# Performance work log

Measured on AMD Instinct MI355X. Metric: run time of the kernel, lower is better.

## Reference

```python
import jax, jax.numpy as jnp
import numpy as np

L = 160        # voxel grid side
BATCH = 4
N_SAMPLE = 62500
N = 64


def _build_coords():
    rng = np.random.default_rng(0)
    coords = []
    for b in range(BATCH):
        c = np.unique(rng.integers(0, L, (N_SAMPLE, 3)), axis=0)  # sorted, unique
        bc = np.concatenate([np.full((len(c), 1), b, dtype=np.int64), c.astype(np.int64)], axis=1)
        coords.append(bc)
    return np.concatenate(coords, axis=0)  # [P,4] = (batch, x, y, z), globally key-sorted


def _neighbor_table(C):
    # integer key per coordinate; coords are unique+sorted so keys are strictly increasing
    keys = ((C[:, 0] * L + C[:, 1]) * L + C[:, 2]) * L + C[:, 3]
    P = C.shape[0]
    offs = np.array([[dx, dy, dz] for dx in (-1, 0, 1) for dy in (-1, 0, 1) for dz in (-1, 0, 1)], dtype=np.int64)
    nbr = np.full((P, 27), -1, dtype=np.int32)
    for k, o in enumerate(offs):
        nc = C[:, 1:] + o
        valid = np.all((nc >= 0) & (nc < L), axis=1)
        nk = ((C[:, 0] * L + nc[:, 0]) * L + nc[:, 1]) * L + nc[:, 2]
        pos = np.clip(np.searchsorted(keys, nk), 0, P - 1)
        found = valid & (keys[pos] == nk)
        nbr[:, k] = np.where(found, pos, -1).astype(np.int32)
    return nbr


def setup_inputs() -> dict:
    C = _build_coords()
    nbr = _neighbor_table(C)
    P = C.shape[0]
    key = jax.random.key(0)
    ks = jax.random.split(key, 10)
    s = 0.05  # small weight scale keeps activations well-conditioned
    return {
        "feats": jax.random.normal(ks[0], (P, N), jnp.float32),
        "cond": jax.random.normal(ks[1], (P, 2 * N), jnp.float32),
        "W1a": jax.random.normal(ks[2], (27, N, N), jnp.float32) * s,
        "b1a": jax.random.normal(ks[3], (N,), jnp.float32) * s,
        "W1b": jax.random.normal(ks[4], (27, N, N), jnp.float32) * s,
        "b1b": jax.random.normal(ks[5], (N,), jnp.float32) * s,
        "W2a": jax.random.normal(ks[6], (27, N, N), jnp.float32) * s,
        "b2a": jax.random.normal(ks[7], (N,), jnp.float32) * s,
        "W2b": jax.random.normal(ks[8], (27, N, N), jnp.float32) * s,
        "b2b": jax.random.normal(ks[9], (N,), jnp.float32) * s,
        "nbr": jnp.asarray(nbr),
    }


def _sparse_conv(x, nbr, W, b):
    # x: [P,N] features, nbr: [P,27] neighbor indices (-1 = missing)
    mask = (nbr >= 0)
    idx = jnp.maximum(nbr, 0)
    acc0 = jnp.zeros((x.shape[0], W.shape[2]), x.dtype)

    def body(acc, kin):
        wk, ik, mk = kin            # wk:[N,N], ik:[P], mk:[P]
        g = x[ik] * mk[:, None].astype(x.dtype)
        return acc + g @ wk, None

    out, _ = jax.lax.scan(body, acc0, (W, idx.T, mask.T))
    return out + b


def reference(feats, cond, W1a, b1a, W1b, b1b, W2a, b2a, W2b, b2b, nbr):
    x_res = feats
    # conv_1: conv -> relu -> conv
    h = _sparse_conv(feats, nbr, W1a, b1a)
    h = jax.nn.relu(h)
    h = _sparse_conv(h, nbr, W1b, b1b)
    # FiLM from condition (features_at_coordinates at identical coords -> direct lookup)
    beta, gamma = jnp.split(cond, 2, axis=1)
    h = h * beta + gamma
    # conv_2: conv -> relu -> conv -> relu
    h = _sparse_conv(h, nbr, W2a, b2a)
    h = jax.nn.relu(h)
    h = _sparse_conv(h, nbr, W2b, b2b)
    h = jax.nn.relu(h)
    # residual: x_res at same coordinates is an identity lookup
    return h + x_res
```

## Files before the change

### kernel.cpp

```cpp
#include <hip/hip_runtime.h>
#include <hip/hip_bf16.h>


#define N 64
#define TAPS 27
#define MT 256

typedef unsigned short u16;
typedef __attribute__((ext_vector_type(8))) short short8;
typedef __attribute__((ext_vector_type(16))) float floatx16;

__device__ __forceinline__ float bf2f(u16 v) {
    union { unsigned u; float f; } c;
    c.u = ((unsigned)v) << 16;
    return c.f;
}
__device__ __forceinline__ u16 f2bf(float f) {
    __hip_bfloat16 h = __float2bfloat16(f);
    u16 r;
    __builtin_memcpy(&r, &h, 2);
    return r;
}
__device__ __forceinline__ void split2(float x, u16& hi, u16& lo) {
    hi = f2bf(x);
    lo = f2bf(x - bf2f(hi));
}

__device__ __forceinline__ void async16(u16* lds, const u16* g) {
    __builtin_amdgcn_global_load_lds(
        (const __attribute__((address_space(1))) unsigned int*)g,
        (__attribute__((address_space(3))) unsigned int*)lds, 16, 0, 0);
}

__global__ void zero_zp(u16* zp) { zp[threadIdx.x] = 0; }

__global__ void split_feats(const float* __restrict__ x, u16* __restrict__ hl, int n) {
    int i = blockIdx.x * 256 + threadIdx.x;
    if (i >= n) return;
    int p = i >> 6, c = i & 63;
    u16 h, l;
    split2(x[i], h, l);
    hl[(size_t)p * 128 + c] = h;
    hl[(size_t)p * 128 + 64 + c] = l;
}

__global__ void transpose_w(const float* __restrict__ W, u16* __restrict__ Wt) {
    const float* src = W + blockIdx.x * (N * N);
    u16* dst = Wt + blockIdx.x * (N * 128);
    int t = threadIdx.x;
#pragma unroll
    for (int m = 0; m < 16; ++m) {
        int e = t + m * 256;
        int i = e >> 6;
        int j = e & 63;
        u16 h, l;
        split2(src[e], h, l);
        int x = (((i >> 3) ^ (j & 7)) * 8) + (i & 7);
        dst[j * 128 + x] = h;
        dst[j * 128 + 64 + x] = l;
    }
}

template <int MODE>
__global__ __launch_bounds__(256, 2) void conv_k(
    const u16* __restrict__ Xhl, const u16* __restrict__ Wt,
    const float* __restrict__ bias, const int* __restrict__ nbr,
    const float* __restrict__ cond, const float* __restrict__ resid,
    const u16* __restrict__ zp,
    u16* __restrict__ out_hl, float* __restrict__ out_f32, int P) {
    __shared__ __align__(16) u16 As[MT * 128];
    __shared__ __align__(16) u16 Bs[N * 128];

    const int tid = threadIdx.x;
    const int pbase = blockIdx.x * MT;

    const int w = tid >> 6;
    const int lane = tid & 63;
    const int cn = lane & 31;
    const int kh = lane >> 5;
    const int rowA0 = w * 64 + cn;

    const int lrow = lane >> 4;
    const int lslot = lane & 15;
    const int swzE = (lslot >> 3) * 64 + (((lslot & 7) ^ lrow) * 8);
    const int swzO = (lslot >> 3) * 64 + (((lslot & 7) ^ (4 + lrow)) * 8);

    floatx16 acc00, acc01, acc10, acc11;
#pragma unroll
    for (int i = 0; i < 16; ++i) { acc00[i] = 0.f; acc01[i] = 0.f; acc10[i] = 0.f; acc11[i] = 0.f; }

    for (int k = 0; k < TAPS; ++k) {
        if (k) __syncthreads();

        int ii[16];
#pragma unroll
        for (int i = 0; i < 16; ++i) {
            const int pr = pbase + w * 64 + i * 4 + lrow;
            const int pc = (pr < P) ? pr : (P - 1);
            int v = nbr[(size_t)pc * TAPS + k];
            ii[i] = (pr < P) ? v : -1;
        }
#pragma unroll
        for (int i = 0; i < 16; ++i) {
            const u16* s = (ii[i] >= 0)
                ? Xhl + (size_t)ii[i] * 128 + ((i & 1) ? swzO : swzE)
                : zp + lslot * 8;
            async16(&As[(w * 64 + i * 4) * 128], s);
        }
        {
            const u16* wk = Wt + ((size_t)k * N + w * 16) * 128 + lane * 8;
#pragma unroll
            for (int q = 0; q < 4; ++q) {
                async16(&Bs[(w * 16 + q * 4) * 128], wk + q * (4 * 128));
            }
        }

        __syncthreads();

#pragma unroll
        for (int kc = 0; kc < 4; ++kc) {
            const int g = 2 * kc + kh;
            const int sw = (g ^ (cn & 7)) * 8;
            const short8 a_h0 = *reinterpret_cast<const short8*>(&As[rowA0 * 128 + sw]);
            const short8 a_l0 = *reinterpret_cast<const short8*>(&As[rowA0 * 128 + 64 + sw]);
            const short8 a_h1 = *reinterpret_cast<const short8*>(&As[(rowA0 + 32) * 128 + sw]);
            const short8 a_l1 = *reinterpret_cast<const short8*>(&As[(rowA0 + 32) * 128 + 64 + sw]);
            const short8 b_h0 = *reinterpret_cast<const short8*>(&Bs[cn * 128 + sw]);
            const short8 b_l0 = *reinterpret_cast<const short8*>(&Bs[cn * 128 + 64 + sw]);
            const short8 b_h1 = *reinterpret_cast<const short8*>(&Bs[(cn + 32) * 128 + sw]);
            const short8 b_l1 = *reinterpret_cast<const short8*>(&Bs[(cn + 32) * 128 + 64 + sw]);

            acc00 = __builtin_amdgcn_mfma_f32_32x32x16_bf16(a_h0, b_h0, acc00, 0, 0, 0);
            acc00 = __builtin_amdgcn_mfma_f32_32x32x16_bf16(a_h0, b_l0, acc00, 0, 0, 0);
            acc00 = __builtin_amdgcn_mfma_f32_32x32x16_bf16(a_l0, b_h0, acc00, 0, 0, 0);

            acc01 = __builtin_amdgcn_mfma_f32_32x32x16_bf16(a_h0, b_h1, acc01, 0, 0, 0);
            acc01 = __builtin_amdgcn_mfma_f32_32x32x16_bf16(a_h0, b_l1, acc01, 0, 0, 0);
            acc01 = __builtin_amdgcn_mfma_f32_32x32x16_bf16(a_l0, b_h1, acc01, 0, 0, 0);

            acc10 = __builtin_amdgcn_mfma_f32_32x32x16_bf16(a_h1, b_h0, acc10, 0, 0, 0);
            acc10 = __builtin_amdgcn_mfma_f32_32x32x16_bf16(a_h1, b_l0, acc10, 0, 0, 0);
            acc10 = __builtin_amdgcn_mfma_f32_32x32x16_bf16(a_l1, b_h0, acc10, 0, 0, 0);

            acc11 = __builtin_amdgcn_mfma_f32_32x32x16_bf16(a_h1, b_h1, acc11, 0, 0, 0);
            acc11 = __builtin_amdgcn_mfma_f32_32x32x16_bf16(a_h1, b_l1, acc11, 0, 0, 0);
            acc11 = __builtin_amdgcn_mfma_f32_32x32x16_bf16(a_l1, b_h1, acc11, 0, 0, 0);
        }
    }

    auto epi = [&](const floatx16& a, int mt, int nt) {
        const int j = nt * 32 + cn;
        const float bj = bias[j];
#pragma unroll
        for (int reg = 0; reg < 16; ++reg) {
            const int row = (reg & 3) + 8 * (reg >> 2) + 4 * kh;
            const int p = pbase + w * 64 + mt * 32 + row;
            if (p < P) {
                float o = a[reg] + bj;
                if (MODE == 0 || MODE == 2) o = fmaxf(o, 0.f);
                if (MODE == 1) {
                    const float be = cond[(size_t)p * (2 * N) + j];
                    const float ga = cond[(size_t)p * (2 * N) + N + j];
                    o = o * be + ga;
                }
                if (MODE == 3) {
                    o = fmaxf(o, 0.f) + resid[(size_t)p * N + j];
                    out_f32[(size_t)p * N + j] = o;
                } else {
                    u16 h, l;
                    split2(o, h, l);
                    out_hl[(size_t)p * 128 + j] = h;
                    out_hl[(size_t)p * 128 + 64 + j] = l;
                }
            }
        }
    };
    epi(acc00, 0, 0);
    epi(acc01, 0, 1);
    epi(acc10, 1, 0);
    epi(acc11, 1, 1);
}

extern "C" void kernel_launch(void* const* d_in, const int* in_sizes, int n_in,
                              void* d_out, int out_size, void* d_ws, size_t ws_size,
                              hipStream_t stream) {
    const float* feats = (const float*)d_in[0];
    const float* cond  = (const float*)d_in[1];
    const float* W1a   = (const float*)d_in[2];
    const float* b1a   = (const float*)d_in[3];
    const float* W1b   = (const float*)d_in[4];
    const float* b1b   = (const float*)d_in[5];
    const float* W2a   = (const float*)d_in[6];
    const float* b2a   = (const float*)d_in[7];
    const float* W2b   = (const float*)d_in[8];
    const float* b2b   = (const float*)d_in[9];
    const int* nbr     = (const int*)d_in[10];
    float* out = (float*)d_out;
    u16* out_hl = (u16*)d_out;

    const int P = in_sizes[0] / N;

    const size_t wtElems = (size_t)TAPS * N * 128;
    u16* zp  = (u16*)d_ws;
    u16* wt0 = zp + 128;
    u16* wt1 = wt0 + wtElems;
    u16* wt2 = wt1 + wtElems;
    u16* wt3 = wt2 + wtElems;
    u16* hA  = wt3 + wtElems;

    zero_zp<<<1, 128, 0, stream>>>(zp);
    transpose_w<<<TAPS, 256, 0, stream>>>(W1a, wt0);
    transpose_w<<<TAPS, 256, 0, stream>>>(W1b, wt1);
    transpose_w<<<TAPS, 256, 0, stream>>>(W2a, wt2);
    transpose_w<<<TAPS, 256, 0, stream>>>(W2b, wt3);
    split_feats<<<(P * N + 255) / 256, 256, 0, stream>>>(feats, out_hl, P * N);

    const int blocks = (P + MT - 1) / MT;
    conv_k<0><<<blocks, 256, 0, stream>>>(out_hl, wt0, b1a, nbr, nullptr, nullptr, zp, hA, nullptr, P);
    conv_k<1><<<blocks, 256, 0, stream>>>(hA, wt1, b1b, nbr, cond, nullptr, zp, out_hl, nullptr, P);
    conv_k<2><<<blocks, 256, 0, stream>>>(out_hl, wt2, b2a, nbr, nullptr, nullptr, zp, hA, nullptr, P);
    conv_k<3><<<blocks, 256, 0, stream>>>(hA, wt3, b2b, nbr, nullptr, feats, zp, nullptr, out, P);
}
```

Measured before the change: 1.116 ms.

## Replace dense 27-tap gather with rulebook sparse pairs plus dense center tap

```diff
diff --git a/kernel.cpp b/kernel.cpp
--- a/kernel.cpp
+++ b/kernel.cpp
@@ -4,7 +4,9 @@
 
 #define N 64
 #define TAPS 27
-#define MT 256
+#define MTD 128
+#define MT2 128
+#define SEGCAP 8192
 
 typedef unsigned short u16;
 typedef __attribute__((ext_vector_type(8))) short short8;
@@ -25,14 +27,26 @@
     hi = f2bf(x);
     lo = f2bf(x - bf2f(hi));
 }
-
 __device__ __forceinline__ void async16(u16* lds, const u16* g) {
     __builtin_amdgcn_global_load_lds(
         (const __attribute__((address_space(1))) unsigned int*)g,
         (__attribute__((address_space(3))) unsigned int*)lds, 16, 0, 0);
 }
 
-__global__ void zero_zp(u16* zp) { zp[threadIdx.x] = 0; }
+__global__ void zero_misc(u16* zp, int* hdr) {
+    const int t = threadIdx.x;
+    zp[t] = 0;
+    if (t < 64) hdr[t] = 0;
+}
+
+__global__ void zero_partial(float* p, const unsigned char* __restrict__ hasSp, int P) {
+    long i = (long)blockIdx.x * 256 + threadIdx.x;
+    const long n4 = (long)P * 16;
+    const long stride = (long)gridDim.x * 256;
+    const float4 z = make_float4(0.f, 0.f, 0.f, 0.f);
+    for (; i < n4; i += stride)
+        if (hasSp[i >> 4]) reinterpret_cast<float4*>(p)[i] = z;
+}
 
 __global__ void split_feats(const float* __restrict__ x, u16* __restrict__ hl, int n) {
     int i = blockIdx.x * 256 + threadIdx.x;
@@ -44,9 +58,12 @@
     hl[(size_t)p * 128 + 64 + c] = l;
 }
 
-__global__ void transpose_w(const float* __restrict__ W, u16* __restrict__ Wt) {
-    const float* src = W + blockIdx.x * (N * N);
-    u16* dst = Wt + blockIdx.x * (N * 128);
+__global__ void transpose_w4(const float* __restrict__ A, const float* __restrict__ B,
+                             const float* __restrict__ C, const float* __restrict__ D,
+                             u16* __restrict__ Wt) {
+    const float* srcs[4] = {A, B, C, D};
+    const float* src = srcs[blockIdx.y] + blockIdx.x * (N * N);
+    u16* dst = Wt + (size_t)blockIdx.y * (TAPS * N * 128) + (size_t)blockIdx.x * (N * 128);
     int t = threadIdx.x;
 #pragma unroll
     for (int m = 0; m < 16; ++m) {
@@ -61,124 +78,240 @@
     }
 }
 
-template <int MODE>
-__global__ __launch_bounds__(256, 2) void conv_k(
+__global__ void build_pairs(const int* __restrict__ nbr, int* __restrict__ hdr,
+                            int* __restrict__ pair_p, int* __restrict__ pair_q,
+                            unsigned char* __restrict__ hasSp, int P) {
+    int p = blockIdx.x * 256 + threadIdx.x;
+    if (p >= P) return;
+    const int* row = nbr + (size_t)p * TAPS;
+    int hs = 0;
+#pragma unroll
+    for (int k = 0; k < TAPS; ++k) {
+        if (k == 13) continue;
+        int q = row[k];
+        if (q >= 0) {
+            hs = 1;
+            int pos = atomicAdd(&hdr[k], 1);
+            if (pos < SEGCAP) {
+                pair_p[k * SEGCAP + pos] = p;
+                pair_q[k * SEGCAP + pos] = q;
+            }
+        }
+    }
+    hasSp[p] = (unsigned char)hs;
+}
+
+__global__ void finalize_pairs(int* __restrict__ hdr, int* __restrict__ c2k,
+                               int* __restrict__ cbase,
+                               int* __restrict__ pair_p, int* __restrict__ pair_q) {
+    __shared__ int soff[28];
+    const int tid = threadIdx.x;
+    if (tid == 0) {
+        int tot = 0;
+        for (int k = 0; k < TAPS; ++k) {
+            int c = hdr[k];
+            if (c > SEGCAP) c = SEGCAP;
+            hdr[k] = c;
+            soff[k] = tot;
+            tot += (c + MT2 - 1) / MT2;
+        }
+        soff[27] = tot;
+        hdr[32] = tot;
+    }
+    __syncthreads();
+    const int tot = soff[27];
+    for (int idx = tid; idx < tot; idx += 256) {
+        int k = 0;
+        while (!(idx >= soff[k] && idx < soff[k + 1])) ++k;
+        c2k[idx] = k;
+        cbase[idx] = k * SEGCAP + (idx - soff[k]) * MT2;
+    }
+    for (int k = 0; k < TAPS; ++k) {
+        const int c = hdr[k];
+        const int e = ((c + MT2 - 1) / MT2) * MT2;
+        for (int j = c + tid; j < e; j += 256) {
+            pair_p[k * SEGCAP + j] = 0;
+            pair_q[k * SEGCAP + j] = -1;
+        }
+    }
+}
+
+__global__ __launch_bounds__(256, 3) void sparse_k(
     const u16* __restrict__ Xhl, const u16* __restrict__ Wt,
-    const float* __restrict__ bias, const int* __restrict__ nbr,
-    const float* __restrict__ cond, const float* __restrict__ resid,
-    const u16* __restrict__ zp,
-    u16* __restrict__ out_hl, float* __restrict__ out_f32, int P) {
-    __shared__ __align__(16) u16 As[MT * 128];
+    const int* __restrict__ pair_p, const int* __restrict__ pair_q,
+    const int* __restrict__ c2k, const int* __restrict__ cbase,
+    const int* __restrict__ hdr, const u16* __restrict__ zp,
+    float* __restrict__ partial) {
+    __shared__ __align__(16) u16 As[MT2 * 128];
     __shared__ __align__(16) u16 Bs[N * 128];
+    __shared__ int pp[MT2];
 
     const int tid = threadIdx.x;
-    const int pbase = blockIdx.x * MT;
-
     const int w = tid >> 6;
     const int lane = tid & 63;
     const int cn = lane & 31;
     const int kh = lane >> 5;
-    const int rowA0 = w * 64 + cn;
-
     const int lrow = lane >> 4;
     const int lslot = lane & 15;
     const int swzE = (lslot >> 3) * 64 + (((lslot & 7) ^ lrow) * 8);
     const int swzO = (lslot >> 3) * 64 + (((lslot & 7) ^ (4 + lrow)) * 8);
-
-    floatx16 acc00, acc01, acc10, acc11;
-#pragma unroll
-    for (int i = 0; i < 16; ++i) { acc00[i] = 0.f; acc01[i] = 0.f; acc10[i] = 0.f; acc11[i] = 0.f; }
-
-    for (int k = 0; k < TAPS; ++k) {
-        if (k) __syncthreads();
-
-        int ii[16];
-#pragma unroll
-        for (int i = 0; i < 16; ++i) {
-            const int pr = pbase + w * 64 + i * 4 + lrow;
-            const int pc = (pr < P) ? pr : (P - 1);
-            int v = nbr[(size_t)pc * TAPS + k];
-            ii[i] = (pr < P) ? v : -1;
-        }
-#pragma unroll
-        for (int i = 0; i < 16; ++i) {
-            const u16* s = (ii[i] >= 0)
-                ? Xhl + (size_t)ii[i] * 128 + ((i & 1) ? swzO : swzE)
-                : zp + lslot * 8;
-            async16(&As[(w * 64 + i * 4) * 128], s);
+    const int rowA = w * 32 + cn;
+
+    const int tc = hdr[32];
+    for (int c = blockIdx.x; c < tc; c += gridDim.x) {
+        if (c != (int)blockIdx.x) __syncthreads();
+        const int k = c2k[c];
+        const int base = cbase[c];
+
+        if (tid < MT2) pp[tid] = pair_p[base + tid];
+#pragma unroll
+        for (int i = 0; i < 8; ++i) {
+            const int q = pair_q[base + w * 32 + i * 4 + lrow];
+            const u16* s = (q >= 0) ? Xhl + (size_t)q * 128 + ((i & 1) ? swzO : swzE)
+                                    : zp + lslot * 8;
+            async16(&As[(w * 32 + i * 4) * 128], s);
         }
         {
             const u16* wk = Wt + ((size_t)k * N + w * 16) * 128 + lane * 8;
 #pragma unroll
-            for (int q = 0; q < 4; ++q) {
-                async16(&Bs[(w * 16 + q * 4) * 128], wk + q * (4 * 128));
-            }
-        }
-
+            for (int q = 0; q < 4; ++q)
+                async16(&Bs[(w * 16 + q * 4) * 128], wk + q * 512);
+        }
         __syncthreads();
 
+        floatx16 acc0, acc1;
+#pragma unroll
+        for (int i = 0; i < 16; ++i) { acc0[i] = 0.f; acc1[i] = 0.f; }
 #pragma unroll
         for (int kc = 0; kc < 4; ++kc) {
             const int g = 2 * kc + kh;
             const int sw = (g ^ (cn & 7)) * 8;
-            const short8 a_h0 = *reinterpret_cast<const short8*>(&As[rowA0 * 128 + sw]);
-            const short8 a_l0 = *reinterpret_cast<const short8*>(&As[rowA0 * 128 + 64 + sw]);
-            const short8 a_h1 = *reinterpret_cast<const short8*>(&As[(rowA0 + 32) * 128 + sw]);
-            const short8 a_l1 = *reinterpret_cast<const short8*>(&As[(rowA0 + 32) * 128 + 64 + sw]);
+            const short8 a_h = *reinterpret_cast<const short8*>(&As[rowA * 128 + sw]);
+            const short8 a_l = *reinterpret_cast<const short8*>(&As[rowA * 128 + 64 + sw]);
             const short8 b_h0 = *reinterpret_cast<const short8*>(&Bs[cn * 128 + sw]);
             const short8 b_l0 = *reinterpret_cast<const short8*>(&Bs[cn * 128 + 64 + sw]);
             const short8 b_h1 = *reinterpret_cast<const short8*>(&Bs[(cn + 32) * 128 + sw]);
             const short8 b_l1 = *reinterpret_cast<const short8*>(&Bs[(cn + 32) * 128 + 64 + sw]);
-
-            acc00 = __builtin_amdgcn_mfma_f32_32x32x16_bf16(a_h0, b_h0, acc00, 0, 0, 0);
-            acc00 = __builtin_amdgcn_mfma_f32_32x32x16_bf16(a_h0, b_l0, acc00, 0, 0, 0);
-            acc00 = __builtin_amdgcn_mfma_f32_32x32x16_bf16(a_l0, b_h0, acc00, 0, 0, 0);
-
-            acc01 = __builtin_amdgcn_mfma_f32_32x32x16_bf16(a_h0, b_h1, acc01, 0, 0, 0);
-            acc01 = __builtin_amdgcn_mfma_f32_32x32x16_bf16(a_h0, b_l1, acc01, 0, 0, 0);
-            acc01 = __builtin_amdgcn_mfma_f32_32x32x16_bf16(a_l0, b_h1, acc01, 0, 0, 0);
-
-            acc10 = __builtin_amdgcn_mfma_f32_32x32x16_bf16(a_h1, b_h0, acc10, 0, 0, 0);
-            acc10 = __builtin_amdgcn_mfma_f32_32x32x16_bf16(a_h1, b_l0, acc10, 0, 0, 0);
-            acc10 = __builtin_amdgcn_mfma_f32_32x32x16_bf16(a_l1, b_h0, acc10, 0, 0, 0);
-
-            acc11 = __builtin_amdgcn_mfma_f32_32x32x16_bf16(a_h1, b_h1, acc11, 0, 0, 0);
-            acc11 = __builtin_amdgcn_mfma_f32_32x32x16_bf16(a_h1, b_l1, acc11, 0, 0, 0);
-            acc11 = __builtin_amdgcn_mfma_f32_32x32x16_bf16(a_l1, b_h1, acc11, 0, 0, 0);
-        }
-    }
-
-    auto epi = [&](const floatx16& a, int mt, int nt) {
-        const int j = nt * 32 + cn;
-        const float bj = bias[j];
+            acc0 = __builtin_amdgcn_mfma_f32_32x32x16_bf16(a_h, b_h0, acc0, 0, 0, 0);
+            acc0 = __builtin_amdgcn_mfma_f32_32x32x16_bf16(a_h, b_l0, acc0, 0, 0, 0);
+            acc0 = __builtin_amdgcn_mfma_f32_32x32x16_bf16(a_l, b_h0, acc0, 0, 0, 0);
+            acc1 = __builtin_amdgcn_mfma_f32_32x32x16_bf16(a_h, b_h1, acc1, 0, 0, 0);
+            acc1 = __builtin_amdgcn_mfma_f32_32x32x16_bf16(a_h, b_l1, acc1, 0, 0, 0);
+            acc1 = __builtin_amdgcn_mfma_f32_32x32x16_bf16(a_l, b_h1, acc1, 0, 0, 0);
+        }
 #pragma unroll
         for (int reg = 0; reg < 16; ++reg) {
             const int row = (reg & 3) + 8 * (reg >> 2) + 4 * kh;
-            const int p = pbase + w * 64 + mt * 32 + row;
-            if (p < P) {
-                float o = a[reg] + bj;
-                if (MODE == 0 || MODE == 2) o = fmaxf(o, 0.f);
-                if (MODE == 1) {
-                    const float be = cond[(size_t)p * (2 * N) + j];
-                    const float ga = cond[(size_t)p * (2 * N) + N + j];
-                    o = o * be + ga;
-                }
-                if (MODE == 3) {
-                    o = fmaxf(o, 0.f) + resid[(size_t)p * N + j];
-                    out_f32[(size_t)p * N + j] = o;
-                } else {
-                    u16 h, l;
-                    split2(o, h, l);
-                    out_hl[(size_t)p * 128 + j] = h;
-                    out_hl[(size_t)p * 128 + 64 + j] = l;
-                }
-            }
-        }
-    };
-    epi(acc00, 0, 0);
-    epi(acc01, 0, 1);
-    epi(acc10, 1, 0);
-    epi(acc11, 1, 1);
+            const int p = pp[w * 32 + row];
+            unsafeAtomicAdd(&partial[(size_t)p * N + cn], acc0[reg]);
+            unsafeAtomicAdd(&partial[(size_t)p * N + 32 + cn], acc1[reg]);
+        }
+    }
+}
+
+template <int MODE>
+__global__ __launch_bounds__(256, 3) void conv_dense(
+    const u16* Xhl, const u16* __restrict__ Wt13,
+    const float* __restrict__ bias, const float* __restrict__ cond,
+    const float* __restrict__ resid, const u16* __restrict__ zp,
+    const unsigned char* __restrict__ hasSp,
+    float* partial, u16* out_hl, float* out_f32, int P) {
+    __shared__ __align__(16) u16 As[MTD * 128];
+    __shared__ __align__(16) u16 Bs[N * 128];
+
+    const int tid = threadIdx.x;
+    const int pbase = blockIdx.x * MTD;
+    const int w = tid >> 6;
+    const int lane = tid & 63;
+    const int cn = lane & 31;
+    const int kh = lane >> 5;
+    const int lrow = lane >> 4;
+    const int lslot = lane & 15;
+    const int swzE = (lslot >> 3) * 64 + (((lslot & 7) ^ lrow) * 8);
+    const int swzO = (lslot >> 3) * 64 + (((lslot & 7) ^ (4 + lrow)) * 8);
+    const int rowA = w * 32 + cn;
+
+#pragma unroll
+    for (int i = 0; i < 8; ++i) {
+        const int pr = pbase + w * 32 + i * 4 + lrow;
+        const u16* s = (pr < P) ? Xhl + (size_t)pr * 128 + ((i & 1) ? swzO : swzE)
+                                : zp + lslot * 8;
+        async16(&As[(w * 32 + i * 4) * 128], s);
+    }
+    {
+        const u16* wk = Wt13 + (size_t)(w * 16) * 128 + lane * 8;
+#pragma unroll
+        for (int q = 0; q < 4; ++q)
+            async16(&Bs[(w * 16 + q * 4) * 128], wk + q * 512);
+    }
+    __syncthreads();
+
+    floatx16 acc0, acc1;
+#pragma unroll
+    for (int i = 0; i < 16; ++i) { acc0[i] = 0.f; acc1[i] = 0.f; }
+
+#pragma unroll
+    for (int kc = 0; kc < 4; ++kc) {
+        const int g = 2 * kc + kh;
+        const int sw = (g ^ (cn & 7)) * 8;
+        const short8 a_h = *reinterpret_cast<const short8*>(&As[rowA * 128 + sw]);
+        const short8 a_l = *reinterpret_cast<const short8*>(&As[rowA * 128 + 64 + sw]);
+        const short8 b_h0 = *reinterpret_cast<const short8*>(&Bs[cn * 128 + sw]);
+        const short8 b_l0 = *reinterpret_cast<const short8*>(&Bs[cn * 128 + 64 + sw]);
+        const short8 b_h1 = *reinterpret_cast<const short8*>(&Bs[(cn + 32) * 128 + sw]);
+        const short8 b_l1 = *reinterpret_cast<const short8*>(&Bs[(cn + 32) * 128 + 64 + sw]);
+        acc0 = __builtin_amdgcn_mfma_f32_32x32x16_bf16(a_h, b_h0, acc0, 0, 0, 0);
+        acc0 = __builtin_amdgcn_mfma_f32_32x32x16_bf16(a_h, b_l0, acc0, 0, 0, 0);
+        acc0 = __builtin_amdgcn_mfma_f32_32x32x16_bf16(a_l, b_h0, acc0, 0, 0, 0);
+        acc1 = __builtin_amdgcn_mfma_f32_32x32x16_bf16(a_h, b_h1, acc1, 0, 0, 0);
+        acc1 = __builtin_amdgcn_mfma_f32_32x32x16_bf16(a_h, b_l1, acc1, 0, 0, 0);
+        acc1 = __builtin_amdgcn_mfma_f32_32x32x16_bf16(a_l, b_h1, acc1, 0, 0, 0);
+    }
+
+#pragma unroll
+    for (int reg = 0; reg < 16; ++reg) {
+        const int row = (reg & 3) + 8 * (reg >> 2) + 4 * kh;
+        const int p = pbase + w * 32 + row;
+        if (p < P && hasSp[p]) {
+            acc0[reg] += partial[(size_t)p * N + cn];
+            acc1[reg] += partial[(size_t)p * N + 32 + cn];
+        }
+    }
+    __syncthreads();
+
+    const float bj0 = bias[cn];
+    const float bj1 = bias[32 + cn];
+#pragma unroll
+    for (int reg = 0; reg < 16; ++reg) {
+        const int row = (reg & 3) + 8 * (reg >> 2) + 4 * kh;
+        const int p = pbase + w * 32 + row;
+        if (p >= P) continue;
+        float o0 = acc0[reg] + bj0;
+        float o1 = acc1[reg] + bj1;
+        if (MODE == 0 || MODE == 2) { o0 = fmaxf(o0, 0.f); o1 = fmaxf(o1, 0.f); }
+        if (MODE == 1) {
+            const float be0 = cond[(size_t)p * 128 + cn];
+            const float ga0 = cond[(size_t)p * 128 + 64 + cn];
+            const float be1 = cond[(size_t)p * 128 + 32 + cn];
+            const float ga1 = cond[(size_t)p * 128 + 96 + cn];
+            o0 = o0 * be0 + ga0;
+            o1 = o1 * be1 + ga1;
+        }
+        if (MODE == 3) {
+            o0 = fmaxf(o0, 0.f) + resid[(size_t)p * N + cn];
+            o1 = fmaxf(o1, 0.f) + resid[(size_t)p * N + 32 + cn];
+            out_f32[(size_t)p * N + cn] = o0;
+            out_f32[(size_t)p * N + 32 + cn] = o1;
+        } else {
+            u16 h, l;
+            split2(o0, h, l);
+            out_hl[(size_t)p * 128 + cn] = h;
+            out_hl[(size_t)p * 128 + 64 + cn] = l;
+            split2(o1, h, l);
+            out_hl[(size_t)p * 128 + 32 + cn] = h;
+            out_hl[(size_t)p * 128 + 96 + cn] = l;
+        }
+    }
 }
 
 extern "C" void kernel_launch(void* const* d_in, const int* in_sizes, int n_in,
@@ -195,29 +328,55 @@
     const float* W2b   = (const float*)d_in[8];
     const float* b2b   = (const float*)d_in[9];
     const int* nbr     = (const int*)d_in[10];
-    float* out = (float*)d_out;
-    u16* out_hl = (u16*)d_out;
 
     const int P = in_sizes[0] / N;
-
-    const size_t wtElems = (size_t)TAPS * N * 128;
-    u16* zp  = (u16*)d_ws;
-    u16* wt0 = zp + 128;
-    u16* wt1 = wt0 + wtElems;
-    u16* wt2 = wt1 + wtElems;
-    u16* wt3 = wt2 + wtElems;
-    u16* hA  = wt3 + wtElems;
-
-    zero_zp<<<1, 128, 0, stream>>>(zp);
-    transpose_w<<<TAPS, 256, 0, stream>>>(W1a, wt0);
-    transpose_w<<<TAPS, 256, 0, stream>>>(W1b, wt1);
-    transpose_w<<<TAPS, 256, 0, stream>>>(W2a, wt2);
-    transpose_w<<<TAPS, 256, 0, stream>>>(W2b, wt3);
-    split_feats<<<(P * N + 255) / 256, 256, 0, stream>>>(feats, out_hl, P * N);
-
-    const int blocks = (P + MT - 1) / MT;
-    conv_k<0><<<blocks, 256, 0, stream>>>(out_hl, wt0, b1a, nbr, nullptr, nullptr, zp, hA, nullptr, P);
-    conv_k<1><<<blocks, 256, 0, stream>>>(hA, wt1, b1b, nbr, cond, nullptr, zp, out_hl, nullptr, P);
-    conv_k<2><<<blocks, 256, 0, stream>>>(out_hl, wt2, b2a, nbr, nullptr, nullptr, zp, hA, nullptr, P);
-    conv_k<3><<<blocks, 256, 0, stream>>>(hA, wt3, b2b, nbr, nullptr, feats, zp, nullptr, out, P);
-}
+    const size_t wtE = (size_t)TAPS * N * 128;
+
+    char* ws = (char*)d_ws;
+    u16* zp = (u16*)ws;        ws += 512;
+    u16* wt = (u16*)ws;        ws += 4 * wtE * sizeof(u16);
+    int* hdr = (int*)ws;       ws += 256;
+    int* c2k = (int*)ws;       ws += 2048 * 4;
+    int* cbase = (int*)ws;     ws += 2048 * 4;
+    int* pair_p = (int*)ws;    ws += (size_t)TAPS * SEGCAP * 4;
+    int* pair_q = (int*)ws;    ws += (size_t)TAPS * SEGCAP * 4;
+    unsigned char* hasSp = (unsigned char*)ws;
+    ws += ((size_t)P + 255) & ~(size_t)255;
+    u16* hA = (u16*)ws;
+
+    u16* wt0 = wt;
+    u16* wt1 = wt + wtE;
+    u16* wt2 = wt + 2 * wtE;
+    u16* wt3 = wt + 3 * wtE;
+    const int T13 = 13 * (N * 128);
+
+    float* pOut = (float*)d_out;
+    u16*   hOut = (u16*)d_out;
+    float* hAf  = (float*)hA;
+
+    zero_misc<<<1, 256, 0, stream>>>(zp, hdr);
+    transpose_w4<<<dim3(TAPS, 4), 256, 0, stream>>>(W1a, W1b, W2a, W2b, wt);
+    split_feats<<<(P * N + 255) / 256, 256, 0, stream>>>(feats, hA, P * N);
+    build_pairs<<<(P + 255) / 256, 256, 0, stream>>>(nbr, hdr, pair_p, pair_q, hasSp, P);
+    finalize_pairs<<<1, 256, 0, stream>>>(hdr, c2k, cbase, pair_p, pair_q);
+
+    const int gd = (P + MTD - 1) / MTD;
+
+    zero_partial<<<1024, 256, 0, stream>>>(pOut, hasSp, P);
+    sparse_k<<<512, 256, 0, stream>>>(hA, wt0, pair_p, pair_q, c2k, cbase, hdr, zp, pOut);
+    conv_dense<0><<<gd, 256, 0, stream>>>(hA, wt0 + T13, b1a, nullptr, nullptr, zp, hasSp, pOut, hOut, nullptr, P);
+
+    zero_partial<<<1024, 256, 0, stream>>>(hAf, hasSp, P);
+    sparse_k<<<512, 256, 0, stream>>>(hOut, wt1, pair_p, pair_q, c2k, cbase, hdr, zp, hAf);
+    conv_dense<1><<<gd, 256, 0, stream>>>(hOut, wt1 + T13, b1b, cond, nullptr, zp, hasSp, hAf, hA, nullptr, P);
+
+    zero_partial<<<1024, 256, 0, stream>>>(pOut, hasSp, P);
+    sparse_k<<<512, 256, 0, stream>>>(hA, wt2, pair_p, pair_q, c2k, cbase, hdr, zp, pOut);
+    conv_dense<2><<<gd, 256, 0, stream>>>(hA, wt2 + T13, b2a, nullptr, nullptr, zp, hasSp, pOut, hOut, nullptr, P);
+
+    zero_partial<<<1024, 256, 0, stream>>>(hAf, hasSp, P);
+    sparse_k<<<512, 256, 0, stream>>>(hOut, wt3, pair_p, pair_q, c2k, cbase, hdr, zp, hAf);
+    conv_dense<3><<<gd, 256, 0, stream>>>(hOut, wt3 + T13, b2b, nullptr, feats, zp, hasSp, hAf, nullptr, pOut, P);
+
+    (void)ws_size; (void)n_in; (void)out_size;
+}
```

Result: slower. 1.639 ms (+46.8%).
